# Optimization experiments

Measured on AMD Instinct MI355X. Metric: run time of the kernel, lower is better.

Reference implementation:

```python
import jax, jax.numpy as jnp
import numpy as np

B, T, C, H = 8, 2048, 1024, 64

def setup_inputs() -> dict:
    key = jax.random.key(0)
    ks = jax.random.split(key, 8)
    s = 1.0 / np.sqrt(C)  # ~Linear init scale
    return {
        "x_real": jax.random.normal(ks[0], (B, T, C), jnp.float32),
        "x_imag": jax.random.normal(ks[1], (B, T, C), jnp.float32),
        "Wk_r": jax.random.normal(ks[2], (C, H), jnp.float32) * s,
        "Wk_i": jax.random.normal(ks[3], (C, H), jnp.float32) * s,
        "Wq_r": jax.random.normal(ks[4], (C, H), jnp.float32) * s,
        "Wq_i": jax.random.normal(ks[5], (C, H), jnp.float32) * s,
        "Wv_r": jax.random.normal(ks[6], (C, H), jnp.float32) * s,
        "Wv_i": jax.random.normal(ks[7], (C, H), jnp.float32) * s,
    }

def _complex_linear(x_real, x_imag, Wr, Wi):
    # (xr + i xi) @ (Wr + i Wi)
    out_real = x_real @ Wr - x_imag @ Wi
    out_imag = x_imag @ Wr + x_real @ Wi
    return out_real, out_imag

def reference(x_real, x_imag, Wk_r, Wk_i, Wq_r, Wq_i, Wv_r, Wv_i):
    k_r, k_i = _complex_linear(x_real, x_imag, Wk_r, Wk_i)
    q_r, q_i = _complex_linear(x_real, x_imag, Wq_r, Wq_i)
    v_r, v_i = _complex_linear(x_real, x_imag, Wv_r, Wv_i)
    # complex scores: q @ conj(k)^T equivalent per source math
    wei_real = jnp.einsum('bqh,bkh->bqk', q_r, k_r) + jnp.einsum('bqh,bkh->bqk', q_i, k_i)
    wei_imag = jnp.einsum('bqh,bkh->bqk', q_i, k_r) - jnp.einsum('bqh,bkh->bqk', q_r, k_i)
    eps = 1e-4
    wei_mag = jnp.sqrt(wei_real**2 + wei_imag**2 + eps) * (H ** -0.5)
    causal = jnp.tril(jnp.ones((T, T), dtype=bool))
    wei_mag = jnp.where(causal, wei_mag, -jnp.inf)
    wei = jax.nn.softmax(wei_mag, axis=-1)  # dropout p=0.0 -> identity
    out_real = jnp.einsum('bqk,bkh->bqh', wei, v_r)
    out_imag = jnp.einsum('bqk,bkh->bqh', wei, v_i)
    return out_real, out_imag
```

## Files before the change

kernel.cpp:

```cpp
#include <hip/hip_runtime.h>
#include <hip/hip_bf16.h>
#include <math.h>

#define BB 8
#define TT 2048
#define CC 1024
#define HH 64
#define NROW (BB*TT)
#define NST (NROW*HH)
#define KK2 2048
#define NN 384
#define GN 256
#define VTP 2080

typedef __attribute__((ext_vector_type(8))) short short8;
typedef __attribute__((ext_vector_type(4))) float f32x4;

static __device__ inline unsigned pk_bf16(float a, float b) {
    __hip_bfloat162 h = __float22bfloat162_rn(make_float2(a, b));
    unsigned u; __builtin_memcpy(&u, &h, 4); return u;
}
static __device__ inline short f2bf_s(float a) {
    __hip_bfloat16 h = __float2bfloat16(a);
    short s; __builtin_memcpy(&s, &h, 2); return s;
}
static __device__ inline short8 neg8(short8 a) {
    short8 r;
    #pragma unroll
    for (int i = 0; i < 8; ++i) r[i] = a[i] ^ (short)0x8000;
    return r;
}

static __device__ inline void async16(const void* g, void* l) {
    __builtin_amdgcn_global_load_lds(
        (const __attribute__((address_space(1))) void*)g,
        (__attribute__((address_space(3))) void*)l,
        16, 0, 0);
}

__global__ __launch_bounds__(256) void prep_kernel(
    const float* __restrict__ Wkr, const float* __restrict__ Wki,
    const float* __restrict__ Wqr, const float* __restrict__ Wqi,
    const float* __restrict__ Wvr, const float* __restrict__ Wvi,
    short* __restrict__ Bt)
{
    const int n = blockIdx.x;
    const int g = n >> 6, h = n & 63;
    const int p = g >> 1;
    const bool im = g & 1;
    const float* Wr = (p == 0) ? Wkr : (p == 1) ? Wqr : Wvr;
    const float* Wi = (p == 0) ? Wki : (p == 1) ? Wqi : Wvi;
    const float* W1 = im ? Wi : Wr;
    const float* W2 = im ? Wr : Wi;
    const float s2 = im ? 1.f : -1.f;

    #pragma unroll
    for (int j = 0; j < 8; ++j) {
        int k = threadIdx.x + 256 * j;
        float v = (k < CC) ? W1[k * HH + h] : s2 * W2[(k - CC) * HH + h];
        Bt[(size_t)n * KK2 + k] = f2bf_s(v);
    }
}

__global__ __launch_bounds__(256) void convert_x(
    const float* __restrict__ xr, const float* __restrict__ xi,
    short* __restrict__ X)
{
    int v = blockIdx.x * 256 + threadIdx.x;
    #pragma unroll
    for (int it = 0; it < 4; ++it, v += 4096 * 256) {
        int row = v >> 8;
        int c8 = v & 255;
        const float* src = (c8 < 128) ? xr : xi;
        int col = (c8 & 127) * 8;
        const float4* p = (const float4*)&src[(size_t)row * CC + col];
        float4 a = p[0], b = p[1];
        uint4 o;
        o.x = pk_bf16(a.x, a.y);
        o.y = pk_bf16(a.z, a.w);
        o.z = pk_bf16(b.x, b.y);
        o.w = pk_bf16(b.z, b.w);
        *(uint4*)&X[(size_t)row * KK2 + c8 * 8] = o;
    }
}

#define LDP 72
#define STP 136

__global__ __launch_bounds__(256) void proj_gemm(
    const short* __restrict__ X,
    const short* __restrict__ Bt,
    short* __restrict__ G, short* __restrict__ VT)
{
    __shared__ __attribute__((aligned(16))) short sAB[128 * 64 + 64 * 64];
    short* sA = sAB;
    short* sB = sAB + 128 * 64;

    const int tid = threadIdx.x;
    const int mbase = blockIdx.x * 128;
    const int comp = blockIdx.y;

    const int wave = tid >> 6, lane = tid & 63;
    const int wr = wave >> 1, wc = wave & 1;
    const int quad = lane >> 4, lm = lane & 15;

    const int lgrp = lane >> 3;
    const int lslot = lane & 7;
    const int scol = ((lslot ^ lgrp) << 4);

    const char* Ag = (const char*)(X + (size_t)mbase * KK2);
    const char* Bg = (const char*)(Bt + (size_t)comp * 64 * KK2);

    f32x4 acc[4][2] = {};

    for (int ks = 0; ks < KK2 / 64; ++ks) {
        #pragma unroll
        for (int i = 0; i < 4; ++i) {
            int q = wave * 4 + i;
            async16(Ag + (size_t)(q * 8 + lgrp) * (KK2 * 2) + ks * 128 + scol,
                    (char*)sA + q * 1024);
        }
        #pragma unroll
        for (int i = 0; i < 2; ++i) {
            int q = wave * 2 + i;
            async16(Bg + (size_t)(q * 8 + lgrp) * (KK2 * 2) + ks * 128 + scol,
                    (char*)sB + q * 1024);
        }
        __syncthreads();

        #pragma unroll
        for (int kk = 0; kk < 2; ++kk) {
            const int cs = (kk * 32 + quad * 8) ^ ((lm & 7) << 3);
            short8 af[4], bf[2];
            #pragma unroll
            for (int mi = 0; mi < 4; ++mi)
                af[mi] = *(const short8*)&sA[(64 * wr + 16 * mi + lm) * 64 + cs];
            #pragma unroll
            for (int ni = 0; ni < 2; ++ni)
                bf[ni] = *(const short8*)&sB[(32 * wc + 16 * ni + lm) * 64 + cs];
            #pragma unroll
            for (int mi = 0; mi < 4; ++mi)
                #pragma unroll
                for (int ni = 0; ni < 2; ++ni)
                    acc[mi][ni] = __builtin_amdgcn_mfma_f32_16x16x32_bf16(
                        af[mi], bf[ni], acc[mi][ni], 0, 0, 0);
        }
        __syncthreads();
    }

    if (comp < 4) {
        short* sG = sAB;
        #pragma unroll
        for (int mi = 0; mi < 4; ++mi)
            #pragma unroll
            for (int ni = 0; ni < 2; ++ni)
                #pragma unroll
                for (int r = 0; r < 4; ++r)
                    sG[(64*wr + 16*mi + quad*4 + r) * LDP + 32*wc + 16*ni + lm] =
                        f2bf_s(acc[mi][ni][r]);
        __syncthreads();
        #pragma unroll
        for (int j = 0; j < 4; ++j) {
            int id = tid + 256 * j;
            int row = id >> 3, c8 = id & 7;
            uint4 v = *(const uint4*)&sG[row * LDP + c8 * 8];
            *(uint4*)&G[(size_t)(mbase + row) * GN + comp*64 + c8*8] = v;
        }
    } else {
        short* sT = sAB;
        const int vcomp = comp - 4;
        const int b = mbase >> 11;
        const int tb = mbase & 2047;
        #pragma unroll
        for (int mi = 0; mi < 4; ++mi)
            #pragma unroll
            for (int ni = 0; ni < 2; ++ni)
                #pragma unroll
                for (int r = 0; r < 4; ++r)
                    sT[(32*wc + 16*ni + lm) * STP + 64*wr + 16*mi + quad*4 + r] =
                        f2bf_s(acc[mi][ni][r]);
        __syncthreads();
        #pragma unroll
        for (int j = 0; j < 4; ++j) {
            int id = tid + 256 * j;
            int h = id >> 4, c = id & 15;
            uint4 v = *(const uint4*)&sT[h * STP + c * 8];
            *(uint4*)&VT[(((size_t)vcomp*BB + b)*64 + h)*VTP + tb + c*8] = v;
        }
    }
}

#define PLDS 72
#define SC2 0.18033688f

__global__ __launch_bounds__(256) void attn_kernel(
    const short* __restrict__ G,
    const short* __restrict__ VT,
    float* __restrict__ out)
{
    __shared__ float comb[4][16][128];
    __shared__ float cmw[4][16], clw[4][16];

    const int tid = threadIdx.x;
    const int wave = tid >> 6, lane = tid & 63;
    const int quad = lane >> 4, lm = lane & 15;
    const int j = (int)(gridDim.x - 1) - (int)blockIdx.x;
    const int b = blockIdx.y;
    const int qbase = j * 16;
    const int nkt = (j >> 2) + 1;

    const short* Qrow = G + ((size_t)(b*TT + qbase + lm)) * GN + 128;
    short8 A1[4], A2[4];
    #pragma unroll
    for (int ks = 0; ks < 4; ++ks)
        A1[ks] = *(const short8*)(Qrow + ks*32 + quad*8);
    A2[0] = A1[2]; A2[1] = A1[3];
    A2[2] = neg8(A1[0]); A2[3] = neg8(A1[1]);

    short8 ones;
    #pragma unroll
    for (int i = 0; i < 8; ++i) ones[i] = (short)0x3F80;

    f32x4 Or[4], Oi[4];
    #pragma unroll
    for (int h = 0; h < 4; ++h)
        #pragma unroll
        for (int r = 0; r < 4; ++r) { Or[h][r] = 0.f; Oi[h][r] = 0.f; }
    f32x4 Ol = {0.f, 0.f, 0.f, 0.f};
    float m[4];
    #pragma unroll
    for (int r = 0; r < 4; ++r) m[r] = -INFINITY;

    short* Pw = (short*)&comb[wave][0][0];
    const short* Vrb = VT + (size_t)b * 64 * VTP;
    const short* Vib = VT + ((size_t)BB + b) * 64 * VTP;

    for (int kt = wave; kt < nkt; kt += 4) {
        const int kb = kt * 64;
        const short* Kt = G + ((size_t)(b*TT + kb)) * GN;

        f32x4 mag[4];
        #pragma unroll
        for (int nt = 0; nt < 4; ++nt) {
            const short* Krow = Kt + (size_t)(nt*16 + lm) * GN;
            short8 Bf[4];
            #pragma unroll
            for (int ks = 0; ks < 4; ++ks)
                Bf[ks] = *(const short8*)(Krow + ks*32 + quad*8);
            f32x4 sr = {0.f,0.f,0.f,0.f}, si = {0.f,0.f,0.f,0.f};
            __builtin_amdgcn_s_setprio(1);
            #pragma unroll
            for (int ks = 0; ks < 4; ++ks) {
                sr = __builtin_amdgcn_mfma_f32_16x16x32_bf16(A1[ks], Bf[ks], sr, 0,0,0);
                si = __builtin_amdgcn_mfma_f32_16x16x32_bf16(A2[ks], Bf[ks], si, 0,0,0);
            }
            __builtin_amdgcn_s_setprio(0);
            int tok = kb + nt*16 + lm;
            #pragma unroll
            for (int r = 0; r < 4; ++r) {
                float v = __builtin_amdgcn_sqrtf(
                              fmaf(sr[r], sr[r], fmaf(si[r], si[r], 1e-4f))) * SC2;
                int qrow = qbase + quad*4 + r;
                mag[nt][r] = (tok > qrow) ? -INFINITY : v;
            }
        }

        float tm[4];
        #pragma unroll
        for (int r = 0; r < 4; ++r)
            tm[r] = fmaxf(fmaxf(mag[0][r], mag[1][r]), fmaxf(mag[2][r], mag[3][r]));
        #pragma unroll
        for (int d = 1; d < 16; d <<= 1)
            #pragma unroll
            for (int r = 0; r < 4; ++r)
                tm[r] = fmaxf(tm[r], __shfl_xor(tm[r], d, 16));

        int need = (tm[0] > m[0] + 8.f) | (tm[1] > m[1] + 8.f) |
                   (tm[2] > m[2] + 8.f) | (tm[3] > m[3] + 8.f);
        if (__any(need)) {
            float al[4];
            #pragma unroll
            for (int r = 0; r < 4; ++r) {
                float mn = fmaxf(m[r], tm[r]);
                al[r] = __builtin_amdgcn_exp2f(m[r] - mn);
                m[r] = mn;
            }
            #pragma unroll
            for (int h = 0; h < 4; ++h)
                #pragma unroll
                for (int r = 0; r < 4; ++r) { Or[h][r] *= al[r]; Oi[h][r] *= al[r]; }
            #pragma unroll
            for (int r = 0; r < 4; ++r) Ol[r] *= al[r];
        }

        #pragma unroll
        for (int nt = 0; nt < 4; ++nt)
            #pragma unroll
            for (int r = 0; r < 4; ++r) {
                float p = __builtin_amdgcn_exp2f(mag[nt][r] - m[r]);
                Pw[(quad*4 + r) * PLDS + nt*16 + lm] = f2bf_s(p);
            }
        short8 Af0 = *(const short8*)&Pw[lm * PLDS + quad*8];
        short8 Af1 = *(const short8*)&Pw[lm * PLDS + 32 + quad*8];

        __builtin_amdgcn_s_setprio(1);
        Ol = __builtin_amdgcn_mfma_f32_16x16x32_bf16(Af0, ones, Ol, 0,0,0);
        Ol = __builtin_amdgcn_mfma_f32_16x16x32_bf16(Af1, ones, Ol, 0,0,0);
        __builtin_amdgcn_s_setprio(0);

        #pragma unroll
        for (int ht = 0; ht < 4; ++ht) {
            const short* vr0 = Vrb + (size_t)(ht*16 + lm) * VTP + kb + quad*8;
            const short* vi0 = Vib + (size_t)(ht*16 + lm) * VTP + kb + quad*8;
            short8 br0 = *(const short8*)(vr0);
            short8 br1 = *(const short8*)(vr0 + 32);
            short8 bi0 = *(const short8*)(vi0);
            short8 bi1 = *(const short8*)(vi0 + 32);
            __builtin_amdgcn_s_setprio(1);
            Or[ht] = __builtin_amdgcn_mfma_f32_16x16x32_bf16(Af0, br0, Or[ht], 0,0,0);
            Or[ht] = __builtin_amdgcn_mfma_f32_16x16x32_bf16(Af1, br1, Or[ht], 0,0,0);
            Oi[ht] = __builtin_amdgcn_mfma_f32_16x16x32_bf16(Af0, bi0, Oi[ht], 0,0,0);
            Oi[ht] = __builtin_amdgcn_mfma_f32_16x16x32_bf16(Af1, bi1, Oi[ht], 0,0,0);
            __builtin_amdgcn_s_setprio(0);
        }
    }

    __syncthreads();

    #pragma unroll
    for (int ht = 0; ht < 4; ++ht)
        #pragma unroll
        for (int r = 0; r < 4; ++r) {
            comb[wave][quad*4 + r][ht*16 + lm]      = Or[ht][r];
            comb[wave][quad*4 + r][64 + ht*16 + lm] = Oi[ht][r];
        }
    if (lm == 0) {
        #pragma unroll
        for (int r = 0; r < 4; ++r) {
            cmw[wave][quad*4 + r] = m[r];
            clw[wave][quad*4 + r] = Ol[r];
        }
    }
    __syncthreads();

    for (int e = tid; e < 16*128; e += 256) {
        int q = e >> 7, h = e & 127;
        float mstar = fmaxf(fmaxf(cmw[0][q], cmw[1][q]), fmaxf(cmw[2][q], cmw[3][q]));
        float osum = 0.f, lsum = 0.f;
        #pragma unroll
        for (int w = 0; w < 4; ++w) {
            float f = __builtin_amdgcn_exp2f(cmw[w][q] - mstar);
            osum = fmaf(f, comb[w][q][h], osum);
            lsum = fmaf(f, clw[w][q], lsum);
        }
        float res = osum / lsum;
        int comp = h >> 6, hh = h & 63;
        out[(size_t)comp * NST + ((size_t)(b*TT + qbase + q)) * HH + hh] = res;
    }
}

extern "C" void kernel_launch(void* const* d_in, const int* in_sizes, int n_in,
                              void* d_out, int out_size, void* d_ws, size_t ws_size,
                              hipStream_t stream)
{
    const float* xr  = (const float*)d_in[0];
    const float* xi  = (const float*)d_in[1];
    const float* Wkr = (const float*)d_in[2];
    const float* Wki = (const float*)d_in[3];
    const float* Wqr = (const float*)d_in[4];
    const float* Wqi = (const float*)d_in[5];
    const float* Wvr = (const float*)d_in[6];
    const float* Wvi = (const float*)d_in[7];

    short* Bt = (short*)d_ws;
    short* G  = (short*)((char*)d_ws + (2u  << 20));
    short* VT = (short*)((char*)d_ws + (11u << 20));
    short* X  = (short*)((char*)d_ws + (16u << 20));
    float* out = (float*)d_out;

    prep_kernel<<<NN, 256, 0, stream>>>(Wkr, Wki, Wqr, Wqi, Wvr, Wvi, Bt);

    convert_x<<<4096, 256, 0, stream>>>(xr, xi, X);

    dim3 g1(NROW / 128, 6);
    proj_gemm<<<g1, 256, 0, stream>>>(X, Bt, G, VT);

    dim3 g3(TT / 16, BB);
    attn_kernel<<<g3, 256, 0, stream>>>(G, VT, out);
}
```

Baseline: 282.8 us.

## Prefetch K and V fragments early and reorder attention grid batch-major

Inside the attention loop, all K fragments for the tile are loaded before any score MFMAs, and the V fragments are loaded right after the scores, before the max/softmax step, so global latency overlaps with compute. The grid is also transposed so consecutive blocks cover different batches at the same query tile, keeping the heaviest causal tiles scheduled first across all batches. This raises register pressure (16 K and 16 V short8 fragments live at once), which may reduce occupancy.

New measurement: 260.0 us. 1.09x faster.

```diff
diff --git a/kernel.cpp b/kernel.cpp
--- a/kernel.cpp
+++ b/kernel.cpp
@@ -204,8 +204,8 @@
     const int tid = threadIdx.x;
     const int wave = tid >> 6, lane = tid & 63;
     const int quad = lane >> 4, lm = lane & 15;
-    const int j = (int)(gridDim.x - 1) - (int)blockIdx.x;
-    const int b = blockIdx.y;
+    const int b = blockIdx.x;
+    const int j = (int)(gridDim.y - 1) - (int)blockIdx.y;
     const int qbase = j * 16;
     const int nkt = (j >> 2) + 1;
 
@@ -239,20 +239,24 @@
         const int kb = kt * 64;
         const short* Kt = G + ((size_t)(b*TT + kb)) * GN;
 
-        f32x4 mag[4];
+        short8 Kf[4][4];
         #pragma unroll
         for (int nt = 0; nt < 4; ++nt) {
             const short* Krow = Kt + (size_t)(nt*16 + lm) * GN;
-            short8 Bf[4];
             #pragma unroll
             for (int ks = 0; ks < 4; ++ks)
-                Bf[ks] = *(const short8*)(Krow + ks*32 + quad*8);
+                Kf[nt][ks] = *(const short8*)(Krow + ks*32 + quad*8);
+        }
+
+        f32x4 mag[4];
+        #pragma unroll
+        for (int nt = 0; nt < 4; ++nt) {
             f32x4 sr = {0.f,0.f,0.f,0.f}, si = {0.f,0.f,0.f,0.f};
             __builtin_amdgcn_s_setprio(1);
             #pragma unroll
             for (int ks = 0; ks < 4; ++ks) {
-                sr = __builtin_amdgcn_mfma_f32_16x16x32_bf16(A1[ks], Bf[ks], sr, 0,0,0);
-                si = __builtin_amdgcn_mfma_f32_16x16x32_bf16(A2[ks], Bf[ks], si, 0,0,0);
+                sr = __builtin_amdgcn_mfma_f32_16x16x32_bf16(A1[ks], Kf[nt][ks], sr, 0,0,0);
+                si = __builtin_amdgcn_mfma_f32_16x16x32_bf16(A2[ks], Kf[nt][ks], si, 0,0,0);
             }
             __builtin_amdgcn_s_setprio(0);
             int tok = kb + nt*16 + lm;
@@ -265,6 +269,17 @@
             }
         }
 
+        short8 Vr[4][2], Vi[4][2];
+        #pragma unroll
+        for (int ht = 0; ht < 4; ++ht) {
+            const short* vr0 = Vrb + (size_t)(ht*16 + lm) * VTP + kb + quad*8;
+            const short* vi0 = Vib + (size_t)(ht*16 + lm) * VTP + kb + quad*8;
+            Vr[ht][0] = *(const short8*)(vr0);
+            Vr[ht][1] = *(const short8*)(vr0 + 32);
+            Vi[ht][0] = *(const short8*)(vi0);
+            Vi[ht][1] = *(const short8*)(vi0 + 32);
+        }
+
         float tm[4];
         #pragma unroll
         for (int r = 0; r < 4; ++r)
@@ -310,17 +325,11 @@
 
         #pragma unroll
         for (int ht = 0; ht < 4; ++ht) {
-            const short* vr0 = Vrb + (size_t)(ht*16 + lm) * VTP + kb + quad*8;
-            const short* vi0 = Vib + (size_t)(ht*16 + lm) * VTP + kb + quad*8;
-            short8 br0 = *(const short8*)(vr0);
-            short8 br1 = *(const short8*)(vr0 + 32);
-            short8 bi0 = *(const short8*)(vi0);
-            short8 bi1 = *(const short8*)(vi0 + 32);
             __builtin_amdgcn_s_setprio(1);
-            Or[ht] = __builtin_amdgcn_mfma_f32_16x16x32_bf16(Af0, br0, Or[ht], 0,0,0);
-            Or[ht] = __builtin_amdgcn_mfma_f32_16x16x32_bf16(Af1, br1, Or[ht], 0,0,0);
-            Oi[ht] = __builtin_amdgcn_mfma_f32_16x16x32_bf16(Af0, bi0, Oi[ht], 0,0,0);
-            Oi[ht] = __builtin_amdgcn_mfma_f32_16x16x32_bf16(Af1, bi1, Oi[ht], 0,0,0);
+            Or[ht] = __builtin_amdgcn_mfma_f32_16x16x32_bf16(Af0, Vr[ht][0], Or[ht], 0,0,0);
+            Or[ht] = __builtin_amdgcn_mfma_f32_16x16x32_bf16(Af1, Vr[ht][1], Or[ht], 0,0,0);
+            Oi[ht] = __builtin_amdgcn_mfma_f32_16x16x32_bf16(Af0, Vi[ht][0], Oi[ht], 0,0,0);
+            Oi[ht] = __builtin_amdgcn_mfma_f32_16x16x32_bf16(Af1, Vi[ht][1], Oi[ht], 0,0,0);
             __builtin_amdgcn_s_setprio(0);
         }
     }
@@ -385,6 +394,6 @@
     dim3 g1(NROW / 128, 6);
     proj_gemm<<<g1, 256, 0, stream>>>(X, Bt, G, VT);
 
-    dim3 g3(TT / 16, BB);
+    dim3 g3(BB, TT / 16);
     attn_kernel<<<g3, 256, 0, stream>>>(G, VT, out);
 }
```
